# Kernel optimization log

Hardware: AMD Instinct MI355X
Metric: run time of the kernel (lower is better)

The kernel has to match this reference:

```python
import jax, jax.numpy as jnp
import numpy as np

DT_MIN, DT_MAX = 0.001, 0.1
CHUNK = 64


def setup_inputs() -> dict:
    key = jax.random.key(0)
    ks = jax.random.split(key, 8)
    b, L, D = 2, 4096, 1024
    d_inner, d_state, nheads, K = 2048, 128, 32, 4
    conv_dim = d_inner + 2 * d_state            # 2304
    d_in_proj = 2 * d_inner + 2 * d_state + nheads  # 4384
    f32 = jnp.float32
    return {
        'x': jax.random.normal(ks[0], (b, L, D), f32),
        'in_proj_w': jax.random.normal(ks[1], (d_in_proj, D), f32) * (D ** -0.5),
        'conv_w': jax.random.normal(ks[2], (conv_dim, K), f32) * 0.3,
        'conv_b': jnp.zeros((conv_dim,), f32),
        'dt_bias': jax.random.normal(ks[3], (nheads,), f32) * 0.5,
        'A_log': jnp.log(jax.random.uniform(ks[4], (nheads,), f32, 1.0, 16.0)),
        'D_skip': jnp.ones((nheads,), f32),
        'norm_w': jnp.ones((d_inner,), f32),
        'out_proj_w': jax.random.normal(ks[5], (D, d_inner), f32) * (d_inner ** -0.5),
        'ln_w': jnp.ones((D,), f32),
        'ln_b': jnp.zeros((D,), f32),
    }


def reference(x, in_proj_w, conv_w, conv_b, dt_bias, A_log, D_skip, norm_w, out_proj_w, ln_w, ln_b):
    b, L, d_model = x.shape
    d_inner = norm_w.shape[0]
    nheads = A_log.shape[0]
    hd = d_inner // nheads                      # headdim = 64
    conv_dim = conv_w.shape[0]
    d_state = (conv_dim - d_inner) // 2
    Q = CHUNK
    c = L // Q

    # ---- Mamba2 in_proj ----
    zxbcdt = jnp.einsum('bld,kd->blk', x, in_proj_w)
    z = zxbcdt[..., :d_inner]                                   # gate
    xBC = zxbcdt[..., d_inner:d_inner + conv_dim]
    dt_raw = zxbcdt[..., d_inner + conv_dim:]                   # (b,L,h)

    # ---- causal depthwise conv1d (kernel 4) + SiLU ----
    K = conv_w.shape[1]
    xp = jnp.pad(xBC, ((0, 0), (K - 1, 0), (0, 0)))
    conv = sum(xp[:, k:k + L, :] * conv_w[:, k] for k in range(K)) + conv_b
    xBC = jax.nn.silu(conv)
    x_ssm = xBC[..., :d_inner]
    Bm = xBC[..., d_inner:d_inner + d_state]                    # (b,L,n)
    Cm = xBC[..., d_inner + d_state:]                           # (b,L,n)

    # ---- bounded dt (sigmoid, per SSMBlock fix) ----
    dt = DT_MIN + (DT_MAX - DT_MIN) * jax.nn.sigmoid(dt_raw + dt_bias)  # (b,L,h)
    A = -jnp.exp(A_log)                                          # (h,)

    # ---- chunked SSD selective scan ----
    xh = x_ssm.reshape(b, c, Q, nheads, hd)
    dtc = dt.reshape(b, c, Q, nheads)
    x_dt = xh * dtc[..., None]
    dA = jnp.einsum('bcqh,h->bhcq', dtc, A)
    Acum = jnp.cumsum(dA, axis=-1)                               # (b,h,c,Q)
    Bc = Bm.reshape(b, c, Q, d_state)
    Cc = Cm.reshape(b, c, Q, d_state)

    # intra-chunk (diagonal blocks)
    seg = Acum[..., :, None] - Acum[..., None, :]                # (b,h,c,Q,Q)
    mask = jnp.tril(jnp.ones((Q, Q), bool))
    Lmat = jnp.exp(jnp.where(mask, seg, -jnp.inf))
    Yd = jnp.einsum('bcqn,bcsn,bhcqs,bcshp->bcqhp', Cc, Bc, Lmat, x_dt)

    # chunk end-states
    decay_states = jnp.exp(Acum[..., -1:] - Acum)                # (b,h,c,Q)
    states = jnp.einsum('bcqn,bhcq,bcqhp->bchpn', Bc, decay_states, x_dt)
    chunk_decay = jnp.exp(Acum[..., -1])                         # (b,h,c)

    def step(carry, inp):
        st, dec = inp
        return dec[..., None, None] * carry + st, carry

    _, prevs = jax.lax.scan(
        step, jnp.zeros((b, nheads, hd, d_state), x.dtype),
        (jnp.moveaxis(states, 1, 0), jnp.moveaxis(chunk_decay, 2, 0)))
    prevs = jnp.moveaxis(prevs, 0, 1)                            # (b,c,h,p,n)

    # inter-chunk contribution
    Yo = jnp.einsum('bcqn,bchpn,bhcq->bcqhp', Cc, prevs, jnp.exp(Acum))

    Y = (Yd + Yo).reshape(b, L, nheads, hd) + D_skip[None, None, :, None] * xh.reshape(b, L, nheads, hd)
    y = Y.reshape(b, L, d_inner)

    # ---- gated RMSNorm + out_proj ----
    y = y * jax.nn.silu(z)
    y = y * jax.lax.rsqrt(jnp.mean(y * y, axis=-1, keepdims=True) + 1e-5) * norm_w
    out = jnp.einsum('bli,di->bld', y, out_proj_w)

    # ---- SSMBlock: LayerNorm + (eval-mode dropout) + residual ----
    mu = jnp.mean(out, axis=-1, keepdims=True)
    var = jnp.mean((out - mu) ** 2, axis=-1, keepdims=True)
    ln = (out - mu) * jax.lax.rsqrt(var + 1e-5) * ln_w + ln_b
    return x + ln
```

## Files before the change

kernel.cpp:

```cpp
#include <hip/hip_runtime.h>
#include <math.h>

#define BSZ     2
#define LEN     4096
#define DMODEL  1024
#define DINNER  2048
#define DSTATE  128
#define NHEADS  32
#define HDIM    64
#define CONVDIM 2304
#define QC      64
#define NCHUNK  64
#define ROWS    (BSZ*LEN)
#define SDIM    (HDIM*DSTATE)
#define PB      136
#define PT      72
#define CGRP    (CONVDIM/8)

typedef __attribute__((ext_vector_type(8))) short short8;
typedef __attribute__((ext_vector_type(4))) float f32x4;

__device__ __forceinline__ float silu_(float x){ return x / (1.0f + expf(-x)); }
__device__ __forceinline__ float sigm_(float x){ return 1.0f / (1.0f + expf(-x)); }
__device__ __forceinline__ float bf2f(unsigned short u){
    return __uint_as_float(((unsigned int)u) << 16);
}
__device__ __forceinline__ unsigned short f2bf(float f){
    unsigned int u = __float_as_uint(f);
    u = (u + 0x7fffu + ((u >> 16) & 1u)) >> 16;
    return (unsigned short)u;
}

__device__ __forceinline__ int swzcol(int row, int col) {
    return ((((col >> 3) ^ (row >> 3)) & 7) << 3) | (col & 7);
}
__device__ __forceinline__ int swzblk(int row, int blk) {
    return (((blk ^ (row >> 3)) & 7) << 3);
}

__device__ __forceinline__ void gload16(const void* g, void* l) {
    __builtin_amdgcn_global_load_lds(
        (const __attribute__((address_space(1))) unsigned int*)g,
        (__attribute__((address_space(3))) unsigned int*)l, 16, 0, 0);
}

__global__ __launch_bounds__(256) void cast_bf16(const float* __restrict__ src,
                                                 unsigned short* __restrict__ dst,
                                                 int n4) {
    const int i = blockIdx.x * 256 + threadIdx.x;
    if (i >= n4) return;
    const float4 v = *(const float4*)(src + (size_t)i * 4);
    ushort4 o;
    o.x = f2bf(v.x); o.y = f2bf(v.y); o.z = f2bf(v.z); o.w = f2bf(v.w);
    *(ushort4*)(dst + (size_t)i * 4) = o;
}

__device__ __forceinline__ void stage_half(const unsigned short* __restrict__ G,
                                           void* ldsbase, int w, int lane,
                                           size_t rowbase, int K, int kt) {
#pragma unroll
    for (int u = 0; u < 2; u++) {
        const int f = w * 128 + u * 64 + lane;
        const int r = f >> 3;
        const int cl = (lane & 7) ^ (lane >> 3);
        gload16(G + rowbase + (size_t)r * K + kt + cl * 8,
                (char*)ldsbase + f * 16);
    }
}

#define WAITV(n) asm volatile("s_waitcnt vmcnt(" #n ")" ::: "memory")
#define LGKM0    asm volatile("s_waitcnt lgkmcnt(0)" ::: "memory")
#define BARRIER  do { asm volatile("" ::: "memory"); \
                      __builtin_amdgcn_s_barrier();  \
                      asm volatile("" ::: "memory"); } while (0)

#define READ_A(dst, half)                                                     \
    _Pragma("unroll")                                                         \
    for (int fr = 0; fr < 4; fr++) {                                          \
        const int r_ = (w & 1) * 64 + fr * 16 + l16;                          \
        _Pragma("unroll")                                                     \
        for (int s = 0; s < 2; s++)                                           \
            dst[fr][s] = *(const short8*)((const char*)&lds[cb][0][half][0]   \
                + r_ * 128 + (((s * 4 + quad) ^ rx7) << 4));                  \
    }
#define READ_B(dst, half)                                                     \
    _Pragma("unroll")                                                         \
    for (int fc = 0; fc < 2; fc++) {                                          \
        const int r_ = (w >> 1) * 32 + fc * 16 + l16;                         \
        _Pragma("unroll")                                                     \
        for (int s = 0; s < 2; s++)                                           \
            dst[fc][s] = *(const short8*)((const char*)&lds[cb][1][half][0]   \
                + r_ * 128 + (((s * 4 + quad) ^ rx7) << 4));                  \
    }
#define MFMA16(g, af, bfv)                                                    \
    __builtin_amdgcn_s_setprio(1);                                            \
    _Pragma("unroll")                                                         \
    for (int s = 0; s < 2; s++)                                               \
        _Pragma("unroll")                                                     \
        for (int fr = 0; fr < 4; fr++)                                        \
            _Pragma("unroll")                                                 \
            for (int fc = 0; fc < 2; fc++)                                    \
                acc[g][fr][fc] = __builtin_amdgcn_mfma_f32_16x16x32_bf16(     \
                    af[fr][s], bfv[fc][s], acc[g][fr][fc], 0, 0, 0);          \
    __builtin_amdgcn_s_setprio(0);

template<bool BF16OUT>
__global__ __launch_bounds__(512, 2) void gemm8p(const unsigned short* __restrict__ A,
                                                 const unsigned short* __restrict__ B,
                                                 void* __restrict__ Cout,
                                                 int N, int K, int gx) {
    __shared__ unsigned short lds[2][2][2][8192];
    const int tid = threadIdx.x;
    const int w = tid >> 6, lane = tid & 63;
    const int quad = lane >> 4, l16 = lane & 15;
    const int rx7 = l16 & 7;

    const int nwg = gridDim.x;
    const int id = blockIdx.x;
    const int q8 = nwg >> 3, r8 = nwg & 7;
    const int xcd = id & 7, idx = id >> 3;
    const int wg = (xcd < r8 ? xcd * (q8 + 1) : r8 * (q8 + 1) + (xcd - r8) * q8) + idx;
    const int m0 = (wg / gx) * 256, n0 = (wg % gx) * 256;

    f32x4 acc[4][4][2];
#pragma unroll
    for (int g = 0; g < 4; g++)
#pragma unroll
        for (int i = 0; i < 4; i++)
#pragma unroll
            for (int j = 0; j < 2; j++) acc[g][i][j] = (f32x4){0.f, 0.f, 0.f, 0.f};

    const int NT = K >> 6;
    stage_half(A, &lds[0][0][0][0], w, lane, (size_t)m0 * K, K, 0);
    stage_half(B, &lds[0][1][0][0], w, lane, (size_t)n0 * K, K, 0);
    stage_half(A, &lds[0][0][1][0], w, lane, (size_t)(m0 + 128) * K, K, 0);
    stage_half(B, &lds[0][1][1][0], w, lane, (size_t)(n0 + 128) * K, K, 0);
    WAITV(4); BARRIER;

    short8 af0[4][2], af1[4][2], bf0[2][2], bf1[2][2];
    int cb = 0;
    for (int t = 0; t < NT - 1; t++) {
        const int kn = (t + 1) * 64;
        const int nb = cb ^ 1;
        READ_A(af0, 0); READ_B(bf0, 0);
        stage_half(A, &lds[nb][0][0][0], w, lane, (size_t)m0 * K, K, kn);
        WAITV(4); BARRIER;
        MFMA16(0, af0, bf0);
        LGKM0; BARRIER;
        READ_A(af1, 1);
        stage_half(B, &lds[nb][1][0][0], w, lane, (size_t)n0 * K, K, kn);
        WAITV(4); BARRIER;
        MFMA16(1, af1, bf0);
        LGKM0; BARRIER;
        READ_B(bf1, 1);
        stage_half(A, &lds[nb][0][1][0], w, lane, (size_t)(m0 + 128) * K, K, kn);
        WAITV(6); BARRIER;
        MFMA16(2, af0, bf1);
        LGKM0; BARRIER;
        stage_half(B, &lds[nb][1][1][0], w, lane, (size_t)(n0 + 128) * K, K, kn);
        WAITV(4); BARRIER;
        MFMA16(3, af1, bf1);
        LGKM0; BARRIER;
        cb = nb;
    }
    WAITV(0); BARRIER;
    READ_A(af0, 0); READ_B(bf0, 0);
    MFMA16(0, af0, bf0);
    READ_A(af1, 1);
    MFMA16(1, af1, bf0);
    READ_B(bf1, 1);
    MFMA16(2, af0, bf1);
    MFMA16(3, af1, bf1);

#pragma unroll
    for (int g = 0; g < 4; g++) {
        const int qm = g & 1, qn = g >> 1;
        const int mb = m0 + qm * 128 + (w & 1) * 64;
        const int nb2 = n0 + qn * 128 + (w >> 1) * 32;
#pragma unroll
        for (int fr = 0; fr < 4; fr++)
#pragma unroll
            for (int fc = 0; fc < 2; fc++) {
                const int n = nb2 + fc * 16 + l16;
#pragma unroll
                for (int rr = 0; rr < 4; rr++) {
                    const int m = mb + fr * 16 + quad * 4 + rr;
                    if (BF16OUT)
                        ((unsigned short*)Cout)[(size_t)m * N + n] = f2bf(acc[g][fr][fc][rr]);
                    else
                        ((float*)Cout)[(size_t)m * N + n] = acc[g][fr][fc][rr];
                }
            }
    }
}

__global__ __launch_bounds__(256) void dtproj_mfma(const unsigned short* __restrict__ A,
                                                   const unsigned short* __restrict__ W,
                                                   const float* __restrict__ bias,
                                                   float* __restrict__ dtb,
                                                   int K) {
    __shared__ unsigned short As[128 * 32];
    __shared__ unsigned short Bs[32 * 32];
    const int tid = threadIdx.x;
    const int wave = tid >> 6, lane = tid & 63;
    const int quad = lane >> 4, l16 = lane & 15;
    const int m0 = blockIdx.x * 128;

    f32x4 acc[2][2];
#pragma unroll
    for (int i = 0; i < 2; i++)
#pragma unroll
        for (int j = 0; j < 2; j++) acc[i][j] = (f32x4){0.f, 0.f, 0.f, 0.f};

    for (int kt = 0; kt < K; kt += 32) {
#pragma unroll
        for (int u = 0; u < 2; u++) {
            const int f = u * 256 + tid;
            const int row = f >> 2, ke = (f & 3) * 8;
            gload16(A + (size_t)(m0 + row) * K + kt + ke, ((char*)As) + f * 16);
        }
        if (tid < 128) {
            const int row = tid >> 2, ke = (tid & 3) * 8;
            gload16(W + (size_t)row * K + kt + ke, ((char*)Bs) + tid * 16);
        }
        __syncthreads();
        short8 af[2], bfr[2];
#pragma unroll
        for (int i = 0; i < 2; i++)
            af[i] = *(const short8*)((const char*)As + (wave * 32 + i * 16 + l16) * 64 + quad * 16);
#pragma unroll
        for (int j = 0; j < 2; j++)
            bfr[j] = *(const short8*)((const char*)Bs + (j * 16 + l16) * 64 + quad * 16);
#pragma unroll
        for (int i = 0; i < 2; i++)
#pragma unroll
            for (int j = 0; j < 2; j++)
                acc[i][j] = __builtin_amdgcn_mfma_f32_16x16x32_bf16(
                    af[i], bfr[j], acc[i][j], 0, 0, 0);
        __syncthreads();
    }
#pragma unroll
    for (int i = 0; i < 2; i++)
#pragma unroll
        for (int j = 0; j < 2; j++) {
            const int h = j * 16 + l16;
            const float bh = bias[h];
#pragma unroll
            for (int r = 0; r < 4; r++) {
                const int m = m0 + wave * 32 + i * 16 + quad * 4 + r;
                dtb[(size_t)m * NHEADS + h] =
                    0.001f + 0.099f * sigm_(acc[i][j][r] + bh);
            }
        }
}

__global__ __launch_bounds__(256) void conv_silu_w(const unsigned short* __restrict__ xbc,
                                                   const float* __restrict__ cw,
                                                   const float* __restrict__ cb,
                                                   unsigned short* __restrict__ xssm,
                                                   unsigned short* __restrict__ Bb,
                                                   unsigned short* __restrict__ Cb) {
    const int idx = blockIdx.x * 256 + threadIdx.x;
    const int g = idx % CGRP;
    const int rowblk = idx / CGRP;
    const long row0 = (long)rowblk * 4;
    const int lbase = (int)(row0 & (LEN - 1));
    const int j0 = g * 8;

    float4 wv[8];
    float cbv[8];
#pragma unroll
    for (int e = 0; e < 8; e++) {
        wv[e] = *(const float4*)(cw + (size_t)(j0 + e) * 4);
        cbv[e] = cb[j0 + e];
    }

    short8 win[4];
    const short8 zero8 = (short8){0, 0, 0, 0, 0, 0, 0, 0};
#pragma unroll
    for (int t = 0; t < 3; t++) {
        const int lr = lbase - 3 + t;
        win[t] = (lr >= 0) ? *(const short8*)(xbc + (row0 - 3 + t) * CONVDIM + j0)
                           : zero8;
    }
#pragma unroll
    for (int i = 0; i < 4; i++) {
        win[3] = *(const short8*)(xbc + (row0 + i) * CONVDIM + j0);
        short8 o;
#pragma unroll
        for (int e = 0; e < 8; e++) {
            float acc = cbv[e];
            acc += bf2f((unsigned short)win[0][e]) * wv[e].x;
            acc += bf2f((unsigned short)win[1][e]) * wv[e].y;
            acc += bf2f((unsigned short)win[2][e]) * wv[e].z;
            acc += bf2f((unsigned short)win[3][e]) * wv[e].w;
            o[e] = (short)f2bf(silu_(acc));
        }
        const long row = row0 + i;
        if (j0 < DINNER)
            *(short8*)(xssm + row * DINNER + j0) = o;
        else if (j0 < DINNER + DSTATE)
            *(short8*)(Bb + row * DSTATE + (j0 - DINNER)) = o;
        else
            *(short8*)(Cb + row * DSTATE + (j0 - DINNER - DSTATE)) = o;
        win[0] = win[1]; win[1] = win[2]; win[2] = win[3];
    }
}

__global__ __launch_bounds__(64) void acum_kernel(const float* __restrict__ dtb,
                                                  const float* __restrict__ A_log,
                                                  float* __restrict__ Acum) {
    const int c = blockIdx.x, h = blockIdx.y, b = blockIdx.z;
    const int q = threadIdx.x;
    const float Av = -expf(A_log[h]);
    float v = dtb[((size_t)b * LEN + c * QC + q) * NHEADS + h] * Av;
#pragma unroll
    for (int off = 1; off < 64; off <<= 1) {
        const float n = __shfl_up(v, off, 64);
        if (q >= off) v += n;
    }
    Acum[(((size_t)b * NHEADS + h) * NCHUNK + c) * QC + q] = v;
}

__global__ __launch_bounds__(256) void chunk_mfma(const unsigned short* __restrict__ xssm,
                                                  const unsigned short* __restrict__ Bb,
                                                  const unsigned short* __restrict__ Cb,
                                                  const float* __restrict__ dtb,
                                                  const float* __restrict__ Acum,
                                                  const float* __restrict__ Dskip,
                                                  unsigned short* __restrict__ Y,
                                                  unsigned short* __restrict__ states) {
    const int c = blockIdx.x, h = blockIdx.y, b = blockIdx.z;
    const int tid = threadIdx.x;
    const int wave = tid >> 6, lane = tid & 63;
    const int quad = lane >> 4, l16 = lane & 15;

    __shared__ __attribute__((aligned(16))) unsigned short Bsh[8704];
    __shared__ __attribute__((aligned(16))) unsigned short Csh[9216];
    __shared__ __attribute__((aligned(16))) unsigned short xTs[4608];
    __shared__ float ac[QC], dts[QC], decs[QC];

    const size_t rowbase = (size_t)b * LEN + c * QC;
    if (tid < QC) {
        ac[tid]  = Acum[(((size_t)b * NHEADS + h) * NCHUNK + c) * QC + tid];
        dts[tid] = dtb[(rowbase + tid) * NHEADS + h];
    }
#pragma unroll
    for (int u = 0; u < 4; u++) {
        const int vi = u * 256 + tid;
        const int s = vi >> 4, n0 = (vi & 15) * 8;
        *(short8*)&Bsh[s * PB + n0] = *(const short8*)(Bb + (rowbase + s) * DSTATE + n0);
        *(short8*)&Csh[s * PB + n0] = *(const short8*)(Cb + (rowbase + s) * DSTATE + n0);
    }
#pragma unroll
    for (int u = 0; u < 2; u++) {
        const int vi = u * 256 + tid;
        const int q = vi >> 3, p0 = (vi & 7) * 8;
        const short8 v = *(const short8*)(xssm + (rowbase + q) * DINNER + h * HDIM + p0);
#pragma unroll
        for (int j = 0; j < 8; j++) {
            const int p = p0 + j;
            xTs[p * PT + swzcol(p, q)] = (unsigned short)v[j];
        }
    }
    __syncthreads();
    if (tid < QC) decs[tid] = expf(ac[QC - 1] - ac[tid]) * dts[tid];

    f32x4 S[4];
#pragma unroll
    for (int j = 0; j < 4; j++) S[j] = (f32x4){0.f, 0.f, 0.f, 0.f};
    const int qa = wave * 16 + l16;
#pragma unroll
    for (int ks = 0; ks < 4; ks++) {
        const short8 a = *(const short8*)&Csh[qa * PB + ks * 32 + quad * 8];
#pragma unroll
        for (int j = 0; j < 4; j++) {
            const short8 bb = *(const short8*)&Bsh[(j * 16 + l16) * PB + ks * 32 + quad * 8];
            S[j] = __builtin_amdgcn_mfma_f32_16x16x32_bf16(a, bb, S[j], 0, 0, 0);
        }
    }
    unsigned short slv[4][4];
#pragma unroll
    for (int j = 0; j < 4; j++)
#pragma unroll
        for (int r = 0; r < 4; r++) {
            const int q = wave * 16 + quad * 4 + r, s = j * 16 + l16;
            const float v = (s <= q) ? S[j][r] * expf(ac[q] - ac[s]) * dts[s] : 0.f;
            slv[j][r] = f2bf(v);
        }
    __syncthreads();

    {
        const int sin = lane & 7;
        const int ng  = lane >> 3;
#pragma unroll
        for (int so = 0; so < 2; so++) {
            const int s = (wave * 2 + so) * 8 + sin;
            const float d = decs[s];
            const int cbk = s >> 3;
#pragma unroll
            for (int nh = 0; nh < 2; nh++) {
                const int noct = ng + 8 * nh;
                const int colphys = (((cbk ^ noct) & 7) << 3) | (s & 7);
#pragma unroll
                for (int j = 0; j < 8; j++) {
                    const int n = noct * 8 + ((j + sin) & 7);
                    Csh[n * PT + colphys] = f2bf(bf2f(Bsh[s * PB + n]) * d);
                }
            }
        }
    }
    __syncthreads();

#pragma unroll
    for (int j = 0; j < 4; j++)
#pragma unroll
        for (int r = 0; r < 4; r++) {
            const int row = wave * 16 + quad * 4 + r;
            const int col = j * 16 + l16;
            Bsh[row * PT + swzcol(row, col)] = slv[j][r];
        }
    __syncthreads();

    f32x4 yd[4];
#pragma unroll
    for (int j = 0; j < 4; j++) yd[j] = (f32x4){0.f, 0.f, 0.f, 0.f};
#pragma unroll
    for (int ks = 0; ks < 2; ks++) {
        const int blk = ks * 4 + quad;
        const short8 a = *(const short8*)&Bsh[qa * PT + swzblk(qa, blk)];
#pragma unroll
        for (int j = 0; j < 4; j++) {
            const int row = j * 16 + l16;
            const short8 xb = *(const short8*)&xTs[row * PT + swzblk(row, blk)];
            yd[j] = __builtin_amdgcn_mfma_f32_16x16x32_bf16(a, xb, yd[j], 0, 0, 0);
        }
    }
    const float Dh = Dskip[h];
#pragma unroll
    for (int j = 0; j < 4; j++)
#pragma unroll
        for (int r = 0; r < 4; r++) {
            const int q = wave * 16 + quad * 4 + r, p = j * 16 + l16;
            const float v = yd[j][r] + Dh * bf2f(xTs[p * PT + swzcol(p, q)]);
            Y[(rowbase + q) * DINNER + h * HDIM + p] = f2bf(v);
        }

    f32x4 st[8];
#pragma unroll
    for (int j = 0; j < 8; j++) st[j] = (f32x4){0.f, 0.f, 0.f, 0.f};
#pragma unroll
    for (int ks = 0; ks < 2; ks++) {
        const int blk = ks * 4 + quad;
        const short8 a = *(const short8*)&xTs[qa * PT + swzblk(qa, blk)];
#pragma unroll
        for (int j = 0; j < 8; j++) {
            const int row = j * 16 + l16;
            const short8 bb = *(const short8*)&Csh[row * PT + swzblk(row, blk)];
            st[j] = __builtin_amdgcn_mfma_f32_16x16x32_bf16(a, bb, st[j], 0, 0, 0);
        }
    }
    const size_t sbase = (((size_t)b * NHEADS + h) * NCHUNK + c) * SDIM;
#pragma unroll
    for (int j = 0; j < 8; j++)
#pragma unroll
        for (int r = 0; r < 4; r++) {
            const int p = wave * 16 + quad * 4 + r, n = j * 16 + l16;
            states[sbase + (size_t)p * DSTATE + n] = f2bf(st[j][r]);
        }
}

__global__ __launch_bounds__(256) void scan_kernel(unsigned short* __restrict__ states,
                                                   const float* __restrict__ Acum) {
    __shared__ float dec[NCHUNK];
    const int bh = blockIdx.y;
    const int pn = blockIdx.x * 256 + threadIdx.x;
    if (threadIdx.x < NCHUNK)
        dec[threadIdx.x] = expf(Acum[((size_t)bh * NCHUNK + threadIdx.x) * QC + (QC - 1)]);
    __syncthreads();
    float carry = 0.f;
    const size_t base = (size_t)bh * NCHUNK * SDIM + pn;
    for (int c = 0; c < NCHUNK; c++) {
        const size_t idx = base + (size_t)c * SDIM;
        const float s = bf2f(states[idx]);
        states[idx] = f2bf(carry);
        carry = dec[c] * carry + s;
    }
}

__global__ __launch_bounds__(256) void yo_mfma(const unsigned short* __restrict__ Cb,
                                               const unsigned short* __restrict__ prevs,
                                               const float* __restrict__ Acum,
                                               unsigned short* __restrict__ Y) {
    const int c = blockIdx.x, h = blockIdx.y, b = blockIdx.z;
    const int tid = threadIdx.x;
    const int wave = tid >> 6, lane = tid & 63;
    const int quad = lane >> 4, l16 = lane & 15;
    __shared__ __attribute__((aligned(16))) unsigned short Csh[8704];
    __shared__ __attribute__((aligned(16))) unsigned short Psh[8704];
    __shared__ float eq[QC];
    const size_t rowbase = (size_t)b * LEN + c * QC;
    const size_t pbase = (((size_t)b * NHEADS + h) * NCHUNK + c) * SDIM;
    if (tid < QC)
        eq[tid] = expf(Acum[(((size_t)b * NHEADS + h) * NCHUNK + c) * QC + tid]);
#pragma unroll
    for (int u = 0; u < 4; u++) {
        const int vi = u * 256 + tid;
        const int r = vi >> 4, n0 = (vi & 15) * 8;
        *(short8*)&Csh[r * PB + n0] = *(const short8*)(Cb + (rowbase + r) * DSTATE + n0);
        *(short8*)&Psh[r * PB + n0] = *(const short8*)(prevs + pbase + (size_t)r * DSTATE + n0);
    }
    __syncthreads();

    f32x4 acc[4];
#pragma unroll
    for (int j = 0; j < 4; j++) acc[j] = (f32x4){0.f, 0.f, 0.f, 0.f};
    const int qa = wave * 16 + l16;
#pragma unroll
    for (int ks = 0; ks < 4; ks++) {
        const short8 a = *(const short8*)&Csh[qa * PB + ks * 32 + quad * 8];
#pragma unroll
        for (int j = 0; j < 4; j++) {
            const short8 bb = *(const short8*)&Psh[(j * 16 + l16) * PB + ks * 32 + quad * 8];
            acc[j] = __builtin_amdgcn_mfma_f32_16x16x32_bf16(a, bb, acc[j], 0, 0, 0);
        }
    }
#pragma unroll
    for (int j = 0; j < 4; j++)
#pragma unroll
        for (int r = 0; r < 4; r++) {
            const int q = wave * 16 + quad * 4 + r, p = j * 16 + l16;
            const size_t off = (rowbase + q) * DINNER + h * HDIM + p;
            Y[off] = f2bf(bf2f(Y[off]) + eq[q] * acc[j][r]);
        }
}

__global__ __launch_bounds__(256) void gate_rms(const unsigned short* __restrict__ Y,
                                                const unsigned short* __restrict__ zbf,
                                                const float* __restrict__ nw,
                                                unsigned short* __restrict__ ybf) {
    const int r = blockIdx.x, tid = threadIdx.x;
    float4 yv[2];
    float ss = 0.f;
#pragma unroll
    for (int u = 0; u < 2; u++) {
        const int col = u * 1024 + tid * 4;
        const ushort4 y4 = *(const ushort4*)(Y + (size_t)r * DINNER + col);
        const ushort4 z4 = *(const ushort4*)(zbf + (size_t)r * DINNER + col);
        float4 y;
        y.x = bf2f(y4.x) * silu_(bf2f(z4.x)); y.y = bf2f(y4.y) * silu_(bf2f(z4.y));
        y.z = bf2f(y4.z) * silu_(bf2f(z4.z)); y.w = bf2f(y4.w) * silu_(bf2f(z4.w));
        yv[u] = y;
        ss += y.x * y.x + y.y * y.y + y.z * y.z + y.w * y.w;
    }
#pragma unroll
    for (int off = 32; off; off >>= 1) ss += __shfl_xor(ss, off, 64);
    __shared__ float red[4];
    if ((tid & 63) == 0) red[tid >> 6] = ss;
    __syncthreads();
    ss = red[0] + red[1] + red[2] + red[3];
    const float scale = rsqrtf(ss / (float)DINNER + 1e-5f);
#pragma unroll
    for (int u = 0; u < 2; u++) {
        const int col = u * 1024 + tid * 4;
        const float4 w4 = *(const float4*)(nw + col);
        ushort4 o;
        o.x = f2bf(yv[u].x * scale * w4.x); o.y = f2bf(yv[u].y * scale * w4.y);
        o.z = f2bf(yv[u].z * scale * w4.z); o.w = f2bf(yv[u].w * scale * w4.w);
        *(ushort4*)(ybf + (size_t)r * DINNER + col) = o;
    }
}

__global__ __launch_bounds__(256) void ln_res(const float* __restrict__ outb,
                                              const float* __restrict__ x,
                                              const float* __restrict__ lw,
                                              const float* __restrict__ lb,
                                              float* __restrict__ out) {
    const int r = blockIdx.x, tid = threadIdx.x;
    const int col = tid * 4;
    const float4 v = *(const float4*)(outb + (size_t)r * DMODEL + col);
    float s = v.x + v.y + v.z + v.w;
    float s2 = v.x * v.x + v.y * v.y + v.z * v.z + v.w * v.w;
#pragma unroll
    for (int off = 32; off; off >>= 1) {
        s += __shfl_xor(s, off, 64);
        s2 += __shfl_xor(s2, off, 64);
    }
    __shared__ float rs[4], rs2[4];
    if ((tid & 63) == 0) { rs[tid >> 6] = s; rs2[tid >> 6] = s2; }
    __syncthreads();
    s = rs[0] + rs[1] + rs[2] + rs[3];
    s2 = rs2[0] + rs2[1] + rs2[2] + rs2[3];
    const float mu = s / (float)DMODEL;
    const float var = s2 / (float)DMODEL - mu * mu;
    const float inv = rsqrtf(var + 1e-5f);
    const float4 xw = *(const float4*)(x + (size_t)r * DMODEL + col);
    const float4 w4 = *(const float4*)(lw + col);
    const float4 b4 = *(const float4*)(lb + col);
    float4 o;
    o.x = xw.x + (v.x - mu) * inv * w4.x + b4.x;
    o.y = xw.y + (v.y - mu) * inv * w4.y + b4.y;
    o.z = xw.z + (v.z - mu) * inv * w4.z + b4.z;
    o.w = xw.w + (v.w - mu) * inv * w4.w + b4.w;
    *(float4*)(out + (size_t)r * DMODEL + col) = o;
}

extern "C" void kernel_launch(void* const* d_in, const int* in_sizes, int n_in,
                              void* d_out, int out_size, void* d_ws, size_t ws_size,
                              hipStream_t stream) {
    const float* x          = (const float*)d_in[0];
    const float* in_proj_w  = (const float*)d_in[1];
    const float* conv_w     = (const float*)d_in[2];
    const float* conv_b     = (const float*)d_in[3];
    const float* dt_bias    = (const float*)d_in[4];
    const float* A_log      = (const float*)d_in[5];
    const float* D_skip     = (const float*)d_in[6];
    const float* norm_w     = (const float*)d_in[7];
    const float* out_proj_w = (const float*)d_in[8];
    const float* ln_w       = (const float*)d_in[9];
    const float* ln_b       = (const float*)d_in[10];
    float* out = (float*)d_out;
    float* ws = (float*)d_ws;

    size_t off = 0;
    unsigned short* zbf     = (unsigned short*)(ws + off); off += (size_t)ROWS * DINNER / 2;
    unsigned short* xssm_bf = (unsigned short*)(ws + off); off += (size_t)ROWS * DINNER / 2;
    unsigned short* uni     = (unsigned short*)(ws + off); off += (size_t)ROWS * CONVDIM / 2;
    unsigned short* Bb_bf   = (unsigned short*)(ws + off); off += (size_t)ROWS * DSTATE / 2;
    unsigned short* Cb_bf   = (unsigned short*)(ws + off); off += (size_t)ROWS * DSTATE / 2;
    float* dtb   = ws + off; off += (size_t)ROWS * NHEADS;
    float* Acum  = ws + off; off += (size_t)BSZ * NHEADS * NCHUNK * QC;
    unsigned short* x_bf  = (unsigned short*)(ws + off); off += (size_t)ROWS * DMODEL / 2;
    unsigned short* wi_bf = (unsigned short*)(ws + off); off += (size_t)4384 * DMODEL / 2;
    unsigned short* wo_bf = (unsigned short*)(ws + off); off += (size_t)DMODEL * DINNER / 2;
    unsigned short* states = (unsigned short*)(ws + off); off += (size_t)BSZ * NHEADS * NCHUNK * SDIM / 2;
    const size_t need_bytes = off * sizeof(float);
    if (ws_size < need_bytes) return;

    unsigned short* xbc_bf = uni;
    unsigned short* Ybf    = uni;
    unsigned short* ybf    = xssm_bf;

    cast_bf16<<<(ROWS * DMODEL / 4 + 255) / 256, 256, 0, stream>>>(x, x_bf, ROWS * DMODEL / 4);
    cast_bf16<<<(4384 * DMODEL / 4 + 255) / 256, 256, 0, stream>>>(in_proj_w, wi_bf, 4384 * DMODEL / 4);
    cast_bf16<<<(DMODEL * DINNER / 4 + 255) / 256, 256, 0, stream>>>(out_proj_w, wo_bf, DMODEL * DINNER / 4);

    gemm8p<true><<<(ROWS / 256) * (DINNER / 256), 512, 0, stream>>>(
        x_bf, wi_bf, zbf, DINNER, DMODEL, DINNER / 256);
    gemm8p<true><<<(ROWS / 256) * (CONVDIM / 256), 512, 0, stream>>>(
        x_bf, wi_bf + (size_t)DINNER * DMODEL, xbc_bf, CONVDIM, DMODEL, CONVDIM / 256);
    dtproj_mfma<<<ROWS / 128, 256, 0, stream>>>(
        x_bf, wi_bf + (size_t)(DINNER + CONVDIM) * DMODEL, dt_bias, dtb, DMODEL);

    conv_silu_w<<<(ROWS / 4) * CGRP / 256, 256, 0, stream>>>(
        xbc_bf, conv_w, conv_b, xssm_bf, Bb_bf, Cb_bf);
    acum_kernel<<<dim3(NCHUNK, NHEADS, BSZ), 64, 0, stream>>>(dtb, A_log, Acum);
    chunk_mfma<<<dim3(NCHUNK, NHEADS, BSZ), 256, 0, stream>>>(
        xssm_bf, Bb_bf, Cb_bf, dtb, Acum, D_skip, Ybf, states);
    scan_kernel<<<dim3(SDIM / 256, BSZ * NHEADS), 256, 0, stream>>>(states, Acum);
    yo_mfma<<<dim3(NCHUNK, NHEADS, BSZ), 256, 0, stream>>>(Cb_bf, states, Acum, Ybf);
    gate_rms<<<ROWS, 256, 0, stream>>>(Ybf, zbf, norm_w, ybf);

    gemm8p<false><<<(ROWS / 256) * (DMODEL / 256), 512, 0, stream>>>(
        ybf, wo_bf, out, DMODEL, DINNER, DMODEL / 256);
    ln_res<<<ROWS, 256, 0, stream>>>(out, x, ln_w, ln_b, out);
}
```

Measured before the change: 428.3 us.

## Deepen GEMM prefetch pipeline and split-K the out_proj GEMM

Restructures the bf16 GEMM main loop to prefetch a full k-tile ahead across both LDS buffers, dropping most per-phase vmcnt waits so global loads overlap MFMA work. It also adds split-K support: the out_proj GEMM (only 128 tiles) runs with two K halves, writing partial sums to a new fp32 workspace that the LayerNorm/residual kernel adds back in. This is meant to fill more CUs on the small output GEMM. It costs extra fp32 traffic for the partial buffer and more loop complexity. Correctness relies on the loop prologue and epilogue matching an even tile count.

```diff
diff --git a/kernel.cpp b/kernel.cpp
--- a/kernel.cpp
+++ b/kernel.cpp
@@ -57,13 +57,13 @@
 
 __device__ __forceinline__ void stage_half(const unsigned short* __restrict__ G,
                                            void* ldsbase, int w, int lane,
-                                           size_t rowbase, int K, int kt) {
+                                           size_t rowbase, int lda, int kcol) {
 #pragma unroll
     for (int u = 0; u < 2; u++) {
         const int f = w * 128 + u * 64 + lane;
         const int r = f >> 3;
         const int cl = (lane & 7) ^ (lane >> 3);
-        gload16(G + rowbase + (size_t)r * K + kt + cl * 8,
+        gload16(G + rowbase + (size_t)r * lda + kcol + cl * 8,
                 (char*)ldsbase + f * 16);
     }
 }
@@ -74,22 +74,22 @@
                       __builtin_amdgcn_s_barrier();  \
                       asm volatile("" ::: "memory"); } while (0)
 
-#define READ_A(dst, half)                                                     \
+#define READ_A(dst, buf, half)                                                \
     _Pragma("unroll")                                                         \
     for (int fr = 0; fr < 4; fr++) {                                          \
         const int r_ = (w & 1) * 64 + fr * 16 + l16;                          \
         _Pragma("unroll")                                                     \
         for (int s = 0; s < 2; s++)                                           \
-            dst[fr][s] = *(const short8*)((const char*)&lds[cb][0][half][0]   \
+            dst[fr][s] = *(const short8*)((const char*)&lds[buf][0][half][0]  \
                 + r_ * 128 + (((s * 4 + quad) ^ rx7) << 4));                  \
     }
-#define READ_B(dst, half)                                                     \
+#define READ_B(dst, buf, half)                                                \
     _Pragma("unroll")                                                         \
     for (int fc = 0; fc < 2; fc++) {                                          \
         const int r_ = (w >> 1) * 32 + fc * 16 + l16;                         \
         _Pragma("unroll")                                                     \
         for (int s = 0; s < 2; s++)                                           \
-            dst[fc][s] = *(const short8*)((const char*)&lds[cb][1][half][0]   \
+            dst[fc][s] = *(const short8*)((const char*)&lds[buf][1][half][0]  \
                 + r_ * 128 + (((s * 4 + quad) ^ rx7) << 4));                  \
     }
 #define MFMA16(g, af, bfv)                                                    \
@@ -107,8 +107,10 @@
 template<bool BF16OUT>
 __global__ __launch_bounds__(512, 2) void gemm8p(const unsigned short* __restrict__ A,
                                                  const unsigned short* __restrict__ B,
-                                                 void* __restrict__ Cout,
-                                                 int N, int K, int gx) {
+                                                 void* __restrict__ C0,
+                                                 void* __restrict__ C1,
+                                                 int N, int Kfull, int Ks,
+                                                 int gx, int nwg1) {
     __shared__ unsigned short lds[2][2][2][8192];
     const int tid = threadIdx.x;
     const int w = tid >> 6, lane = tid & 63;
@@ -120,7 +122,16 @@
     const int q8 = nwg >> 3, r8 = nwg & 7;
     const int xcd = id & 7, idx = id >> 3;
     const int wg = (xcd < r8 ? xcd * (q8 + 1) : r8 * (q8 + 1) + (xcd - r8) * q8) + idx;
-    const int m0 = (wg / gx) * 256, n0 = (wg % gx) * 256;
+    const int sid = wg / nwg1;
+    const int wgl = wg % nwg1;
+    const int m0 = (wgl / gx) * 256, n0 = (wgl % gx) * 256;
+    const int kbase = sid * Ks;
+    void* Cout = sid ? C1 : C0;
+
+    const size_t a0r = (size_t)m0 * Kfull;
+    const size_t a1r = (size_t)(m0 + 128) * Kfull;
+    const size_t b0r = (size_t)n0 * Kfull;
+    const size_t b1r = (size_t)(n0 + 128) * Kfull;
 
     f32x4 acc[4][4][2];
 #pragma unroll
@@ -130,45 +141,58 @@
 #pragma unroll
             for (int j = 0; j < 2; j++) acc[g][i][j] = (f32x4){0.f, 0.f, 0.f, 0.f};
 
-    const int NT = K >> 6;
-    stage_half(A, &lds[0][0][0][0], w, lane, (size_t)m0 * K, K, 0);
-    stage_half(B, &lds[0][1][0][0], w, lane, (size_t)n0 * K, K, 0);
-    stage_half(A, &lds[0][0][1][0], w, lane, (size_t)(m0 + 128) * K, K, 0);
-    stage_half(B, &lds[0][1][1][0], w, lane, (size_t)(n0 + 128) * K, K, 0);
-    WAITV(4); BARRIER;
+    const int NT = Ks >> 6;
+    stage_half(A, &lds[0][0][0][0], w, lane, a0r, Kfull, kbase);
+    stage_half(B, &lds[0][1][0][0], w, lane, b0r, Kfull, kbase);
+    stage_half(A, &lds[0][0][1][0], w, lane, a1r, Kfull, kbase);
+    stage_half(B, &lds[0][1][1][0], w, lane, b1r, Kfull, kbase);
+    stage_half(A, &lds[1][0][0][0], w, lane, a0r, Kfull, kbase + 64);
+    stage_half(B, &lds[1][1][0][0], w, lane, b0r, Kfull, kbase + 64);
+    stage_half(A, &lds[1][0][1][0], w, lane, a1r, Kfull, kbase + 64);
+    WAITV(6); BARRIER;
 
     short8 af0[4][2], af1[4][2], bf0[2][2], bf1[2][2];
-    int cb = 0;
-    for (int t = 0; t < NT - 1; t++) {
-        const int kn = (t + 1) * 64;
-        const int nb = cb ^ 1;
-        READ_A(af0, 0); READ_B(bf0, 0);
-        stage_half(A, &lds[nb][0][0][0], w, lane, (size_t)m0 * K, K, kn);
-        WAITV(4); BARRIER;
-        MFMA16(0, af0, bf0);
-        LGKM0; BARRIER;
-        READ_A(af1, 1);
-        stage_half(B, &lds[nb][1][0][0], w, lane, (size_t)n0 * K, K, kn);
-        WAITV(4); BARRIER;
-        MFMA16(1, af1, bf0);
-        LGKM0; BARRIER;
-        READ_B(bf1, 1);
-        stage_half(A, &lds[nb][0][1][0], w, lane, (size_t)(m0 + 128) * K, K, kn);
-        WAITV(6); BARRIER;
-        MFMA16(2, af0, bf1);
-        LGKM0; BARRIER;
-        stage_half(B, &lds[nb][1][1][0], w, lane, (size_t)(n0 + 128) * K, K, kn);
-        WAITV(4); BARRIER;
-        MFMA16(3, af1, bf1);
-        LGKM0; BARRIER;
-        cb = nb;
-    }
-    WAITV(0); BARRIER;
-    READ_A(af0, 0); READ_B(bf0, 0);
+    for (int p = 0; p < (NT >> 1) - 1; p++) {
+        const int kb1 = kbase + (2 * p + 1) * 64;
+        const int ka2 = kbase + (2 * p + 2) * 64;
+        const int kb2 = kbase + (2 * p + 3) * 64;
+        READ_A(af0, 0, 0); READ_B(bf0, 0, 0);
+        stage_half(B, &lds[1][1][1][0], w, lane, b1r, Kfull, kb1);
+        BARRIER; MFMA16(0, af0, bf0); LGKM0; BARRIER;
+        READ_A(af1, 0, 1);
+        stage_half(A, &lds[0][0][0][0], w, lane, a0r, Kfull, ka2);
+        BARRIER; MFMA16(1, af1, bf0); LGKM0; BARRIER;
+        READ_B(bf1, 0, 1);
+        stage_half(B, &lds[0][1][0][0], w, lane, b0r, Kfull, ka2);
+        BARRIER; MFMA16(2, af0, bf1); LGKM0; BARRIER;
+        stage_half(A, &lds[0][0][1][0], w, lane, a1r, Kfull, ka2);
+        WAITV(6); BARRIER; MFMA16(3, af1, bf1); LGKM0; BARRIER;
+        READ_A(af0, 1, 0); READ_B(bf0, 1, 0);
+        stage_half(B, &lds[0][1][1][0], w, lane, b1r, Kfull, ka2);
+        BARRIER; MFMA16(0, af0, bf0); LGKM0; BARRIER;
+        READ_A(af1, 1, 1);
+        stage_half(A, &lds[1][0][0][0], w, lane, a0r, Kfull, kb2);
+        BARRIER; MFMA16(1, af1, bf0); LGKM0; BARRIER;
+        READ_B(bf1, 1, 1);
+        stage_half(B, &lds[1][1][0][0], w, lane, b0r, Kfull, kb2);
+        BARRIER; MFMA16(2, af0, bf1); LGKM0; BARRIER;
+        stage_half(A, &lds[1][0][1][0], w, lane, a1r, Kfull, kb2);
+        WAITV(6); BARRIER; MFMA16(3, af1, bf1); LGKM0; BARRIER;
+    }
+    READ_A(af0, 0, 0); READ_B(bf0, 0, 0);
+    stage_half(B, &lds[1][1][1][0], w, lane, b1r, Kfull, kbase + (NT - 1) * 64);
     MFMA16(0, af0, bf0);
-    READ_A(af1, 1);
+    READ_A(af1, 0, 1);
     MFMA16(1, af1, bf0);
-    READ_B(bf1, 1);
+    READ_B(bf1, 0, 1);
+    MFMA16(2, af0, bf1);
+    MFMA16(3, af1, bf1);
+    WAITV(0); LGKM0; BARRIER;
+    READ_A(af0, 1, 0); READ_B(bf0, 1, 0);
+    MFMA16(0, af0, bf0);
+    READ_A(af1, 1, 1);
+    MFMA16(1, af1, bf0);
+    READ_B(bf1, 1, 1);
     MFMA16(2, af0, bf1);
     MFMA16(3, af1, bf1);
 
@@ -572,13 +596,16 @@
 }
 
 __global__ __launch_bounds__(256) void ln_res(const float* __restrict__ outb,
+                                              const float* __restrict__ part,
                                               const float* __restrict__ x,
                                               const float* __restrict__ lw,
                                               const float* __restrict__ lb,
                                               float* __restrict__ out) {
     const int r = blockIdx.x, tid = threadIdx.x;
     const int col = tid * 4;
-    const float4 v = *(const float4*)(outb + (size_t)r * DMODEL + col);
+    float4 v = *(const float4*)(outb + (size_t)r * DMODEL + col);
+    const float4 pv = *(const float4*)(part + (size_t)r * DMODEL + col);
+    v.x += pv.x; v.y += pv.y; v.z += pv.z; v.w += pv.w;
     float s = v.x + v.y + v.z + v.w;
     float s2 = v.x * v.x + v.y * v.y + v.z * v.z + v.w * v.w;
 #pragma unroll
@@ -634,6 +661,7 @@
     unsigned short* wi_bf = (unsigned short*)(ws + off); off += (size_t)4384 * DMODEL / 2;
     unsigned short* wo_bf = (unsigned short*)(ws + off); off += (size_t)DMODEL * DINNER / 2;
     unsigned short* states = (unsigned short*)(ws + off); off += (size_t)BSZ * NHEADS * NCHUNK * SDIM / 2;
+    float* part = ws + off; off += (size_t)ROWS * DMODEL;
     const size_t need_bytes = off * sizeof(float);
     if (ws_size < need_bytes) return;
 
@@ -646,9 +674,11 @@
     cast_bf16<<<(DMODEL * DINNER / 4 + 255) / 256, 256, 0, stream>>>(out_proj_w, wo_bf, DMODEL * DINNER / 4);
 
     gemm8p<true><<<(ROWS / 256) * (DINNER / 256), 512, 0, stream>>>(
-        x_bf, wi_bf, zbf, DINNER, DMODEL, DINNER / 256);
+        x_bf, wi_bf, zbf, nullptr, DINNER, DMODEL, DMODEL,
+        DINNER / 256, (ROWS / 256) * (DINNER / 256));
     gemm8p<true><<<(ROWS / 256) * (CONVDIM / 256), 512, 0, stream>>>(
-        x_bf, wi_bf + (size_t)DINNER * DMODEL, xbc_bf, CONVDIM, DMODEL, CONVDIM / 256);
+        x_bf, wi_bf + (size_t)DINNER * DMODEL, xbc_bf, nullptr, CONVDIM, DMODEL, DMODEL,
+        CONVDIM / 256, (ROWS / 256) * (CONVDIM / 256));
     dtproj_mfma<<<ROWS / 128, 256, 0, stream>>>(
         x_bf, wi_bf + (size_t)(DINNER + CONVDIM) * DMODEL, dt_bias, dtb, DMODEL);
 
@@ -661,7 +691,8 @@
     yo_mfma<<<dim3(NCHUNK, NHEADS, BSZ), 256, 0, stream>>>(Cb_bf, states, Acum, Ybf);
     gate_rms<<<ROWS, 256, 0, stream>>>(Ybf, zbf, norm_w, ybf);
 
-    gemm8p<false><<<(ROWS / 256) * (DMODEL / 256), 512, 0, stream>>>(
-        ybf, wo_bf, out, DMODEL, DINNER, DMODEL / 256);
-    ln_res<<<ROWS, 256, 0, stream>>>(out, x, ln_w, ln_b, out);
-}
+    gemm8p<false><<<2 * (ROWS / 256) * (DMODEL / 256), 512, 0, stream>>>(
+        ybf, wo_bf, out, part, DMODEL, DINNER, DINNER / 2,
+        DMODEL / 256, (ROWS / 256) * (DMODEL / 256));
+    ln_res<<<ROWS, 256, 0, stream>>>(out, part, x, ln_w, ln_b, out);
+}
```

After: 423.3 us. No clear change (-1.2%).
